# Optimization experiments

Hardware: AMD Instinct MI355X
Metric: run time of the kernel (lower is better)

The kernel has to match this reference:

```python
import jax, jax.numpy as jnp
import numpy as np

L, B, D, N = 4096, 4, 1024, 16


def setup_inputs() -> dict:
    key = jax.random.key(0)
    ks = jax.random.split(key, 6)
    x = jax.random.normal(ks[0], (L, B, D), dtype=jnp.float32)
    delta = 0.2 * jax.random.normal(ks[1], (D, N, 1), dtype=jnp.float32)
    alpha = 0.2 * jax.random.normal(ks[2], (D, N, 1), dtype=jnp.float32)
    # beta init: N(0, 0.02) + 1.0 (val is all ones since i % 1 == 0 always)
    beta = 0.02 * jax.random.normal(ks[3], (D, N, 1), dtype=jnp.float32) + 1.0
    gamma = jax.random.normal(ks[4], (D, N), dtype=jnp.float32)
    omega = jax.random.normal(ks[5], (D,), dtype=jnp.float32)
    return {"x": x, "delta": delta, "alpha": alpha, "beta": beta,
            "gamma": gamma, "omega": omega}


def reference(x, delta, alpha, beta, gamma, omega):
    seq_len = x.shape[0]
    scale = (1.0 / gamma.shape[1]) ** 0.5
    # EMA coefficients
    p = jax.nn.sigmoid(delta)                      # (D, N, 1)
    q = 1.0 - p * jax.nn.sigmoid(alpha)            # (D, N, 1)
    # Vandermonde kernel: k[d, l] = sum_n p*beta * q^l * gamma*scale
    t = jnp.arange(seq_len, dtype=x.dtype)         # (L,)
    vander = t[None, None, :] * jnp.log(q)         # (D, N, L)
    kernel = p * beta * jnp.exp(vander)            # (D, N, L)
    k = jnp.einsum('dnl,dn->dl', kernel, gamma * scale)  # (D, L)
    # Residual path
    residual = x * omega                           # (L, B, D)
    # FFT causal convolution along time
    xt = jnp.transpose(x, (1, 2, 0))               # (B, D, L)
    n_fft = 2 * seq_len
    k_f = jnp.fft.rfft(k.astype(jnp.float32), n=n_fft)      # (D, n_fft//2+1)
    x_f = jnp.fft.rfft(xt.astype(jnp.float32), n=n_fft)     # (B, D, n_fft//2+1)
    out = jnp.fft.irfft(x_f * k_f, n=n_fft)[..., :seq_len]  # (B, D, L)
    out = out.astype(x.dtype)
    out = jax.nn.silu(jnp.transpose(out, (2, 0, 1)) + residual)  # (L, B, D)
    return out
```

## Files before the change

kernel.cpp:

```cpp
#include <hip/hip_runtime.h>
#include <math.h>

#define L_SEQ 4096
#define B_SZ 4
#define D_SZ 1024
#define N_MODES 16
#define CH (B_SZ * D_SZ)
#define ROW (B_SZ * D_SZ)

__global__ void ema_params_kernel(const float* __restrict__ delta,
                                  const float* __restrict__ alpha,
                                  const float* __restrict__ beta,
                                  const float* __restrict__ gamma,
                                  float* __restrict__ qArr,
                                  float* __restrict__ wArr,
                                  float* __restrict__ qLcArr,
                                  int log2Lc) {
    int i = blockIdx.x * blockDim.x + threadIdx.x;
    if (i >= D_SZ * N_MODES) return;
    int d = i / N_MODES;
    int n = i - d * N_MODES;
    float p  = 1.0f / (1.0f + expf(-delta[i]));
    float sa = 1.0f / (1.0f + expf(-alpha[i]));
    float q  = 1.0f - p * sa;
    const float scale = 0.25f;
    float w = p * beta[i] * gamma[i] * scale;
    float qp = q;
    for (int t = 0; t < log2Lc; ++t) qp *= qp;
    int o = n * D_SZ + d;
    qArr[o]   = q;
    wArr[o]   = w;
    qLcArr[o] = qp;
}

__global__ __launch_bounds__(256) void ema_phase1(const float* __restrict__ x,
                                                  const float* __restrict__ qArr,
                                                  float* __restrict__ S,
                                                  int Lc) {
    int tid = threadIdx.x;
    int c = blockIdx.y * 256 + tid;
    int j = blockIdx.x;
    int d = c & (D_SZ - 1);
    float q[N_MODES], h[N_MODES];
#pragma unroll
    for (int n = 0; n < N_MODES; ++n) { q[n] = qArr[n * D_SZ + d]; h[n] = 0.0f; }
    const float* xp = x + (size_t)j * Lc * ROW + c;
    for (int s = 0; s < Lc; ++s) {
        float xv = xp[(size_t)s * ROW];
#pragma unroll
        for (int n = 0; n < N_MODES; ++n) h[n] = fmaf(q[n], h[n], xv);
    }
    float4* Sp = (float4*)(S + ((size_t)j * CH + c) * N_MODES);
#pragma unroll
    for (int r = 0; r < 4; ++r)
        Sp[r] = make_float4(h[4*r], h[4*r+1], h[4*r+2], h[4*r+3]);
}

__global__ __launch_bounds__(256) void ema_phase2(float* __restrict__ S,
                                                  const float* __restrict__ qLcArr,
                                                  int C) {
    int g = blockIdx.x * 256 + threadIdx.x;
    int c = g >> 4;
    int n = g & 15;
    int d = c & (D_SZ - 1);
    float qLc = qLcArr[n * D_SZ + d];
    float carry = 0.0f;
    for (int j = 0; j < C; ++j) {
        size_t idx = (size_t)j * (CH * N_MODES) + g;
        float s = S[idx];
        S[idx] = carry;
        carry = fmaf(qLc, carry, s);
    }
}

__global__ __launch_bounds__(256) void ema_phase3(const float* __restrict__ x,
                                                  const float* __restrict__ qArr,
                                                  const float* __restrict__ wArr,
                                                  const float* __restrict__ S,
                                                  const float* __restrict__ omega,
                                                  float* __restrict__ out,
                                                  int Lc) {
    int tid = threadIdx.x;
    int c = blockIdx.y * 256 + tid;
    int j = blockIdx.x;
    int d = c & (D_SZ - 1);
    float om = omega[d];
    float q[N_MODES], w[N_MODES], h[N_MODES];
    const float4* Sp = (const float4*)(S + ((size_t)j * CH + c) * N_MODES);
#pragma unroll
    for (int r = 0; r < 4; ++r) {
        float4 v = Sp[r];
        h[4*r] = v.x; h[4*r+1] = v.y; h[4*r+2] = v.z; h[4*r+3] = v.w;
    }
#pragma unroll
    for (int n = 0; n < N_MODES; ++n) {
        q[n] = qArr[n * D_SZ + d];
        w[n] = wArr[n * D_SZ + d];
    }
    size_t base = (size_t)j * Lc * ROW + c;
    for (int s = 0; s < Lc; ++s) {
        size_t idx = base + (size_t)s * ROW;
        float xv = x[idx];
        float y0 = 0.0f, y1 = 0.0f, y2 = 0.0f, y3 = 0.0f;
#pragma unroll
        for (int n = 0; n < N_MODES; n += 4) {
            h[n]   = fmaf(q[n],   h[n],   xv); y0 = fmaf(w[n],   h[n],   y0);
            h[n+1] = fmaf(q[n+1], h[n+1], xv); y1 = fmaf(w[n+1], h[n+1], y1);
            h[n+2] = fmaf(q[n+2], h[n+2], xv); y2 = fmaf(w[n+2], h[n+2], y2);
            h[n+3] = fmaf(q[n+3], h[n+3], xv); y3 = fmaf(w[n+3], h[n+3], y3);
        }
        float z = (y0 + y1) + (y2 + y3) + xv * om;
        out[idx] = z / (1.0f + __expf(-z));
    }
}

extern "C" void kernel_launch(void* const* d_in, const int* in_sizes, int n_in,
                              void* d_out, int out_size, void* d_ws, size_t ws_size,
                              hipStream_t stream) {
    const float* x     = (const float*)d_in[0];
    const float* delta = (const float*)d_in[1];
    const float* alpha = (const float*)d_in[2];
    const float* beta  = (const float*)d_in[3];
    const float* gamma = (const float*)d_in[4];
    const float* omega = (const float*)d_in[5];
    float* out = (float*)d_out;

    const size_t paramFloats = (size_t)N_MODES * D_SZ;
    const size_t paramBytes  = paramFloats * sizeof(float);

    int C = 64;
    while (C > 1 &&
           3 * paramBytes + (size_t)C * CH * N_MODES * sizeof(float) > ws_size)
        C >>= 1;
    int Lc = L_SEQ / C;
    int log2Lc = 0;
    while ((1 << log2Lc) < Lc) ++log2Lc;

    float* qArr   = (float*)d_ws;
    float* wArr   = qArr   + paramFloats;
    float* qLcArr = wArr   + paramFloats;
    float* S      = qLcArr + paramFloats;

    ema_params_kernel<<<(D_SZ * N_MODES + 255) / 256, 256, 0, stream>>>(
        delta, alpha, beta, gamma, qArr, wArr, qLcArr, log2Lc);

    dim3 grid(C, CH / 256);
    ema_phase1<<<grid, 256, 0, stream>>>(x, qArr, S, Lc);
    ema_phase2<<<(CH * N_MODES) / 256, 256, 0, stream>>>(S, qLcArr, C);
    ema_phase3<<<grid, 256, 0, stream>>>(x, qArr, wArr, S, omega, out, Lc);
}
```

Measured before the change: 200.2 us.

## Fuse EMA scan phases into one cooperative kernel with wave-shuffle carry scan

Replaces the param kernel and three scan-phase launches with a single cooperative kernel that uses grid-wide syncs between the chunk-local scan, the carry propagation and the output pass. The carry pass becomes a log-step wave shuffle scan across the 64 chunks instead of a sequential loop over chunks. Coefficients are recomputed inline in each phase rather than read from a precomputed workspace, x loads are batched eight at a time, and outputs use nontemporal stores. This removes launch gaps and the serial carry loop, but depends on all 1024 blocks being co-resident and hardcodes the chunk count and workspace size. If the occupancy check fails it falls back to three separate launches.

```diff
diff --git a/kernel.cpp b/kernel.cpp
--- a/kernel.cpp
+++ b/kernel.cpp
@@ -1,117 +1,183 @@
 #include <hip/hip_runtime.h>
+#include <hip/hip_cooperative_groups.h>
 #include <math.h>
 
-#define L_SEQ 4096
-#define B_SZ 4
+namespace cg = cooperative_groups;
+
 #define D_SZ 1024
 #define N_MODES 16
-#define CH (B_SZ * D_SZ)
-#define ROW (B_SZ * D_SZ)
-
-__global__ void ema_params_kernel(const float* __restrict__ delta,
-                                  const float* __restrict__ alpha,
-                                  const float* __restrict__ beta,
-                                  const float* __restrict__ gamma,
-                                  float* __restrict__ qArr,
-                                  float* __restrict__ wArr,
-                                  float* __restrict__ qLcArr,
-                                  int log2Lc) {
-    int i = blockIdx.x * blockDim.x + threadIdx.x;
-    if (i >= D_SZ * N_MODES) return;
-    int d = i / N_MODES;
-    int n = i - d * N_MODES;
-    float p  = 1.0f / (1.0f + expf(-delta[i]));
-    float sa = 1.0f / (1.0f + expf(-alpha[i]));
-    float q  = 1.0f - p * sa;
-    const float scale = 0.25f;
-    float w = p * beta[i] * gamma[i] * scale;
-    float qp = q;
-    for (int t = 0; t < log2Lc; ++t) qp *= qp;
-    int o = n * D_SZ + d;
-    qArr[o]   = q;
-    wArr[o]   = w;
-    qLcArr[o] = qp;
-}
-
-__global__ __launch_bounds__(256) void ema_phase1(const float* __restrict__ x,
-                                                  const float* __restrict__ qArr,
-                                                  float* __restrict__ S,
-                                                  int Lc) {
-    int tid = threadIdx.x;
-    int c = blockIdx.y * 256 + tid;
-    int j = blockIdx.x;
+#define CH 4096
+#define ROW 4096
+#define C_CHUNKS 64
+#define LC 64
+
+__device__ __forceinline__ void load16(const float* __restrict__ p, int d, float v[16]) {
+    const float4* p4 = (const float4*)(p + (size_t)d * 16);
+#pragma unroll
+    for (int r = 0; r < 4; ++r) {
+        float4 t = p4[r];
+        v[4*r+0] = t.x; v[4*r+1] = t.y; v[4*r+2] = t.z; v[4*r+3] = t.w;
+    }
+}
+
+__device__ __forceinline__ void compute_qw(const float* __restrict__ delta,
+                                           const float* __restrict__ alpha,
+                                           const float* __restrict__ beta,
+                                           const float* __restrict__ gamma,
+                                           int d, float q[16], float w[16]) {
+    float dl[16], al[16], bt[16], gm[16];
+    load16(delta, d, dl); load16(alpha, d, al);
+    load16(beta, d, bt);  load16(gamma, d, gm);
+#pragma unroll
+    for (int n = 0; n < 16; ++n) {
+        float p  = 1.0f / (1.0f + __expf(-dl[n]));
+        float sa = 1.0f / (1.0f + __expf(-al[n]));
+        q[n] = 1.0f - p * sa;
+        w[n] = p * bt[n] * gm[n] * 0.25f;
+    }
+}
+
+__device__ __forceinline__ void phase1_body(const float* __restrict__ x, float* __restrict__ S,
+    const float* __restrict__ delta, const float* __restrict__ alpha,
+    const float* __restrict__ beta, const float* __restrict__ gamma, int j, int c) {
     int d = c & (D_SZ - 1);
-    float q[N_MODES], h[N_MODES];
-#pragma unroll
-    for (int n = 0; n < N_MODES; ++n) { q[n] = qArr[n * D_SZ + d]; h[n] = 0.0f; }
-    const float* xp = x + (size_t)j * Lc * ROW + c;
-    for (int s = 0; s < Lc; ++s) {
-        float xv = xp[(size_t)s * ROW];
-#pragma unroll
-        for (int n = 0; n < N_MODES; ++n) h[n] = fmaf(q[n], h[n], xv);
-    }
-    float4* Sp = (float4*)(S + ((size_t)j * CH + c) * N_MODES);
+    float q[16], w[16];
+    compute_qw(delta, alpha, beta, gamma, d, q, w);
+    float h[16];
+#pragma unroll
+    for (int n = 0; n < 16; ++n) h[n] = 0.0f;
+    const float* xp = x + (size_t)j * (LC * ROW) + c;
+#pragma unroll 2
+    for (int s0 = 0; s0 < LC; s0 += 8) {
+        float xv[8];
+#pragma unroll
+        for (int u = 0; u < 8; ++u) xv[u] = xp[(size_t)(s0 + u) * ROW];
+#pragma unroll
+        for (int u = 0; u < 8; ++u)
+#pragma unroll
+            for (int n = 0; n < 16; ++n) h[n] = fmaf(q[n], h[n], xv[u]);
+    }
+    float4* Sp = (float4*)(S + ((size_t)j * CH + c) * 16);
 #pragma unroll
     for (int r = 0; r < 4; ++r)
         Sp[r] = make_float4(h[4*r], h[4*r+1], h[4*r+2], h[4*r+3]);
 }
 
-__global__ __launch_bounds__(256) void ema_phase2(float* __restrict__ S,
-                                                  const float* __restrict__ qLcArr,
-                                                  int C) {
-    int g = blockIdx.x * 256 + threadIdx.x;
-    int c = g >> 4;
-    int n = g & 15;
+__device__ __forceinline__ void phase2_body(float* __restrict__ S,
+    const float* __restrict__ delta, const float* __restrict__ alpha, int c2, int lane) {
+    int d = c2 & (D_SZ - 1);
+    float dl[16], al[16];
+    load16(delta, d, dl); load16(alpha, d, al);
+    float pw[16];
+#pragma unroll
+    for (int n = 0; n < 16; ++n) {
+        float p  = 1.0f / (1.0f + __expf(-dl[n]));
+        float sa = 1.0f / (1.0f + __expf(-al[n]));
+        float qn = 1.0f - p * sa;
+#pragma unroll
+        for (int t = 0; t < 6; ++t) qn *= qn;
+        pw[n] = qn;
+    }
+    float hh[16];
+    float4* Sp = (float4*)(S + ((size_t)lane * CH + c2) * 16);
+#pragma unroll
+    for (int r = 0; r < 4; ++r) {
+        float4 t = Sp[r];
+        hh[4*r] = t.x; hh[4*r+1] = t.y; hh[4*r+2] = t.z; hh[4*r+3] = t.w;
+    }
+#pragma unroll
+    for (int k = 1; k <= 32; k <<= 1) {
+        float prev[16];
+#pragma unroll
+        for (int n = 0; n < 16; ++n) prev[n] = __shfl_up(hh[n], (unsigned)k, 64);
+#pragma unroll
+        for (int n = 0; n < 16; ++n) hh[n] = (lane >= k) ? fmaf(pw[n], prev[n], hh[n]) : hh[n];
+#pragma unroll
+        for (int n = 0; n < 16; ++n) pw[n] *= pw[n];
+    }
+    float cin[16];
+#pragma unroll
+    for (int n = 0; n < 16; ++n) {
+        float t = __shfl_up(hh[n], 1u, 64);
+        cin[n] = (lane == 0) ? 0.0f : t;
+    }
+#pragma unroll
+    for (int r = 0; r < 4; ++r)
+        Sp[r] = make_float4(cin[4*r], cin[4*r+1], cin[4*r+2], cin[4*r+3]);
+}
+
+__device__ __forceinline__ void phase3_body(const float* __restrict__ x,
+    const float* __restrict__ S, float* __restrict__ out,
+    const float* __restrict__ delta, const float* __restrict__ alpha,
+    const float* __restrict__ beta, const float* __restrict__ gamma,
+    const float* __restrict__ omega, int j, int c) {
     int d = c & (D_SZ - 1);
-    float qLc = qLcArr[n * D_SZ + d];
-    float carry = 0.0f;
-    for (int j = 0; j < C; ++j) {
-        size_t idx = (size_t)j * (CH * N_MODES) + g;
-        float s = S[idx];
-        S[idx] = carry;
-        carry = fmaf(qLc, carry, s);
-    }
-}
-
-__global__ __launch_bounds__(256) void ema_phase3(const float* __restrict__ x,
-                                                  const float* __restrict__ qArr,
-                                                  const float* __restrict__ wArr,
-                                                  const float* __restrict__ S,
-                                                  const float* __restrict__ omega,
-                                                  float* __restrict__ out,
-                                                  int Lc) {
+    float q[16], w[16];
+    compute_qw(delta, alpha, beta, gamma, d, q, w);
+    float om = omega[d];
+    float h[16];
+    const float4* Sp = (const float4*)(S + ((size_t)j * CH + c) * 16);
+#pragma unroll
+    for (int r = 0; r < 4; ++r) {
+        float4 t = Sp[r];
+        h[4*r] = t.x; h[4*r+1] = t.y; h[4*r+2] = t.z; h[4*r+3] = t.w;
+    }
+    size_t base = (size_t)j * (LC * ROW) + c;
+#pragma unroll 2
+    for (int s0 = 0; s0 < LC; s0 += 8) {
+        float xv[8];
+#pragma unroll
+        for (int u = 0; u < 8; ++u) xv[u] = x[base + (size_t)(s0 + u) * ROW];
+#pragma unroll
+        for (int u = 0; u < 8; ++u) {
+            float xu = xv[u];
+            float y0 = 0.0f, y1 = 0.0f, y2 = 0.0f, y3 = 0.0f;
+#pragma unroll
+            for (int n = 0; n < 16; n += 4) {
+                h[n]   = fmaf(q[n],   h[n],   xu); y0 = fmaf(w[n],   h[n],   y0);
+                h[n+1] = fmaf(q[n+1], h[n+1], xu); y1 = fmaf(w[n+1], h[n+1], y1);
+                h[n+2] = fmaf(q[n+2], h[n+2], xu); y2 = fmaf(w[n+2], h[n+2], y2);
+                h[n+3] = fmaf(q[n+3], h[n+3], xu); y3 = fmaf(w[n+3], h[n+3], y3);
+            }
+            float z = (y0 + y1) + (y2 + y3) + xu * om;
+            float r = z / (1.0f + __expf(-z));
+            __builtin_nontemporal_store(r, &out[base + (size_t)(s0 + u) * ROW]);
+        }
+    }
+}
+
+__global__ __launch_bounds__(256, 4) void ema_fused(
+    const float* __restrict__ x, const float* __restrict__ delta,
+    const float* __restrict__ alpha, const float* __restrict__ beta,
+    const float* __restrict__ gamma, const float* __restrict__ omega,
+    float* __restrict__ S, float* __restrict__ out) {
     int tid = threadIdx.x;
+    int j = blockIdx.x;
     int c = blockIdx.y * 256 + tid;
-    int j = blockIdx.x;
-    int d = c & (D_SZ - 1);
-    float om = omega[d];
-    float q[N_MODES], w[N_MODES], h[N_MODES];
-    const float4* Sp = (const float4*)(S + ((size_t)j * CH + c) * N_MODES);
-#pragma unroll
-    for (int r = 0; r < 4; ++r) {
-        float4 v = Sp[r];
-        h[4*r] = v.x; h[4*r+1] = v.y; h[4*r+2] = v.z; h[4*r+3] = v.w;
-    }
-#pragma unroll
-    for (int n = 0; n < N_MODES; ++n) {
-        q[n] = qArr[n * D_SZ + d];
-        w[n] = wArr[n * D_SZ + d];
-    }
-    size_t base = (size_t)j * Lc * ROW + c;
-    for (int s = 0; s < Lc; ++s) {
-        size_t idx = base + (size_t)s * ROW;
-        float xv = x[idx];
-        float y0 = 0.0f, y1 = 0.0f, y2 = 0.0f, y3 = 0.0f;
-#pragma unroll
-        for (int n = 0; n < N_MODES; n += 4) {
-            h[n]   = fmaf(q[n],   h[n],   xv); y0 = fmaf(w[n],   h[n],   y0);
-            h[n+1] = fmaf(q[n+1], h[n+1], xv); y1 = fmaf(w[n+1], h[n+1], y1);
-            h[n+2] = fmaf(q[n+2], h[n+2], xv); y2 = fmaf(w[n+2], h[n+2], y2);
-            h[n+3] = fmaf(q[n+3], h[n+3], xv); y3 = fmaf(w[n+3], h[n+3], y3);
-        }
-        float z = (y0 + y1) + (y2 + y3) + xv * om;
-        out[idx] = z / (1.0f + __expf(-z));
-    }
+    phase1_body(x, S, delta, alpha, beta, gamma, j, c);
+    cg::this_grid().sync();
+    int gb = blockIdx.y * gridDim.x + blockIdx.x;
+    phase2_body(S, delta, alpha, gb * 4 + (tid >> 6), tid & 63);
+    cg::this_grid().sync();
+    phase3_body(x, S, out, delta, alpha, beta, gamma, omega, j, c);
+}
+
+__global__ __launch_bounds__(256) void k_phase1(const float* __restrict__ x, float* __restrict__ S,
+    const float* __restrict__ delta, const float* __restrict__ alpha,
+    const float* __restrict__ beta, const float* __restrict__ gamma) {
+    phase1_body(x, S, delta, alpha, beta, gamma, blockIdx.x, blockIdx.y * 256 + threadIdx.x);
+}
+__global__ __launch_bounds__(256) void k_phase2(float* __restrict__ S,
+    const float* __restrict__ delta, const float* __restrict__ alpha) {
+    phase2_body(S, delta, alpha, blockIdx.x * 4 + (threadIdx.x >> 6), threadIdx.x & 63);
+}
+__global__ __launch_bounds__(256) void k_phase3(const float* __restrict__ x,
+    const float* __restrict__ S, float* __restrict__ out,
+    const float* __restrict__ delta, const float* __restrict__ alpha,
+    const float* __restrict__ beta, const float* __restrict__ gamma,
+    const float* __restrict__ omega) {
+    phase3_body(x, S, out, delta, alpha, beta, gamma, omega,
+                blockIdx.x, blockIdx.y * 256 + threadIdx.x);
 }
 
 extern "C" void kernel_launch(void* const* d_in, const int* in_sizes, int n_in,
@@ -124,28 +190,21 @@
     const float* gamma = (const float*)d_in[4];
     const float* omega = (const float*)d_in[5];
     float* out = (float*)d_out;
-
-    const size_t paramFloats = (size_t)N_MODES * D_SZ;
-    const size_t paramBytes  = paramFloats * sizeof(float);
-
-    int C = 64;
-    while (C > 1 &&
-           3 * paramBytes + (size_t)C * CH * N_MODES * sizeof(float) > ws_size)
-        C >>= 1;
-    int Lc = L_SEQ / C;
-    int log2Lc = 0;
-    while ((1 << log2Lc) < Lc) ++log2Lc;
-
-    float* qArr   = (float*)d_ws;
-    float* wArr   = qArr   + paramFloats;
-    float* qLcArr = wArr   + paramFloats;
-    float* S      = qLcArr + paramFloats;
-
-    ema_params_kernel<<<(D_SZ * N_MODES + 255) / 256, 256, 0, stream>>>(
-        delta, alpha, beta, gamma, qArr, wArr, qLcArr, log2Lc);
-
-    dim3 grid(C, CH / 256);
-    ema_phase1<<<grid, 256, 0, stream>>>(x, qArr, S, Lc);
-    ema_phase2<<<(CH * N_MODES) / 256, 256, 0, stream>>>(S, qLcArr, C);
-    ema_phase3<<<grid, 256, 0, stream>>>(x, qArr, wArr, S, omega, out, Lc);
-}
+    float* S   = (float*)d_ws;
+
+    dim3 grid(C_CHUNKS, CH / 256);
+
+    int maxBlocks = 0;
+    hipError_t e = hipOccupancyMaxActiveBlocksPerMultiprocessor(
+        &maxBlocks, (const void*)ema_fused, 256, 0);
+    if (e == hipSuccess && maxBlocks >= 4) {
+        void* args[] = {(void*)&x, (void*)&delta, (void*)&alpha, (void*)&beta,
+                        (void*)&gamma, (void*)&omega, (void*)&S, (void*)&out};
+        hipLaunchCooperativeKernel((const void*)ema_fused, grid, dim3(256, 1, 1),
+                                   args, 0, stream);
+    } else {
+        k_phase1<<<grid, 256, 0, stream>>>(x, S, delta, alpha, beta, gamma);
+        k_phase2<<<CH / 4, 256, 0, stream>>>(S, delta, alpha);
+        k_phase3<<<grid, 256, 0, stream>>>(x, S, out, delta, alpha, beta, gamma, omega);
+    }
+}
```

New measurement: 164.5 us. 17.9% less time.
